# Optimization experiments

Measured on AMD Instinct MI355X. Metric: run time of the kernel, lower is better.

Reference implementation:

```python
import jax, jax.numpy as jnp
import numpy as np

E = 8            # n_expert
K = 2            # n_expert_per_token
C = 2048         # n_embd
I = 1408         # moe_intermediate_size
IS = I * 2       # shared expert intermediate (n_shared_expert=2)
B, T = 2, 2048


def setup_inputs() -> dict:
    key = jax.random.key(0)
    ks = jax.random.split(key, 9)
    s = 0.02
    return {
        "x": jax.random.normal(ks[0], (B, T, C), dtype=jnp.float32),
        "gate_w": jax.random.normal(ks[1], (E, C), dtype=jnp.float32) * s,
        # expert MLP weights, torch Linear convention (out_features, in_features)
        "w1": jax.random.normal(ks[2], (E, I, C), dtype=jnp.float32) * s,  # fc_1
        "w2": jax.random.normal(ks[3], (E, I, C), dtype=jnp.float32) * s,  # fc_2
        "w3": jax.random.normal(ks[4], (E, C, I), dtype=jnp.float32) * s,  # proj
        # shared expert
        "sw1": jax.random.normal(ks[5], (IS, C), dtype=jnp.float32) * s,
        "sw2": jax.random.normal(ks[6], (IS, C), dtype=jnp.float32) * s,
        "sw3": jax.random.normal(ks[7], (C, IS), dtype=jnp.float32) * s,
    }


def reference(x, gate_w, w1, w2, w3, sw1, sw2, sw3):
    Bq, Tq, Cq = x.shape
    xf = x.reshape(-1, Cq)  # [N, C], N = B*T

    # top-k routing: softmax in fp32, then top-k probs per token
    logits = xf @ gate_w.T                                   # [N, E]
    probs = jax.nn.softmax(logits.astype(jnp.float32), axis=-1)
    topk_p, topk_i = jax.lax.top_k(probs, K)                 # [N, K]
    # combine weights: comb[n, e] = sum_k topk_p[n,k] * (topk_i[n,k] == e)
    comb = (jax.nn.one_hot(topk_i, E, dtype=jnp.float32)
            * topk_p[..., None]).sum(axis=1).astype(x.dtype)  # [N, E]

    # per-expert gated-SiLU MLP (batched over experts via einsum)
    h1 = jnp.einsum('nc,eic->eni', xf, w1)                   # [E, N, I]
    h2 = jnp.einsum('nc,eic->eni', xf, w2)                   # [E, N, I]
    h = jax.nn.silu(h1) * h2
    eo = jnp.einsum('eni,eci->enc', h, w3)                   # [E, N, C]

    # weighted scatter-combine
    y = jnp.einsum('enc,ne->nc', eo, comb).reshape(Bq, Tq, Cq)

    # shared expert on the residual input
    sh = (jax.nn.silu(xf @ sw1.T) * (xf @ sw2.T)) @ sw3.T    # [N, C]
    return y + sh.reshape(Bq, Tq, Cq)
```

## Files before the change

kernel.cpp:

```cpp
#include <hip/hip_runtime.h>
#include <stdint.h>

#define N_TOK 4096
#define CDIM  2048
#define NEXP  8
#define IDIM  1408
#define ISDIM 2816
#define CAP   2048
#define ICAT  2816
#define SCAT  5632

typedef __attribute__((ext_vector_type(8))) short bf16x8;
typedef __attribute__((ext_vector_type(4))) float f32x4;

#define GLOAD16(gp, lp) __builtin_amdgcn_global_load_lds( \
    (const __attribute__((address_space(1))) void*)(gp),  \
    (__attribute__((address_space(3))) void*)(lp), 16, 0, 0)

__device__ __forceinline__ unsigned short f2bf(float f) {
  union { float f; unsigned u; } c; c.f = f;
  return (unsigned short)((c.u + 0x7FFFu + ((c.u >> 16) & 1u)) >> 16);
}
__device__ __forceinline__ float bf2f(unsigned short h) {
  union { unsigned u; float f; } c; c.u = (unsigned)h << 16;
  return c.f;
}

__device__ __forceinline__ int xcd_swizzle(int orig, int nwg) {
  int q = nwg >> 3, r = nwg & 7;
  int xcd = orig & 7, idx = orig >> 3;
  return (xcd < r ? xcd * (q + 1) : r * (q + 1) + (xcd - r) * q) + idx;
}

__global__ __launch_bounds__(256) void cvt_all(
    const float* __restrict__ x, const float* __restrict__ w1,
    const float* __restrict__ w2, const float* __restrict__ w3,
    const float* __restrict__ sw1, const float* __restrict__ sw2,
    const float* __restrict__ sw3,
    unsigned short* __restrict__ xb, unsigned short* __restrict__ wcat,
    unsigned short* __restrict__ w3b, unsigned short* __restrict__ swcat,
    unsigned short* __restrict__ sw3b) {
  const int b = blockIdx.x;
  const int t = threadIdx.x;
  const float* src;
  unsigned short* dst;
  if (b < 4096) {
    src = x + (size_t)b * 2048;  dst = xb + (size_t)b * 2048;
  } else if (b < 15360) {
    size_t o = (size_t)(b - 4096) * 2048;  src = w3 + o;  dst = w3b + o;
  } else if (b < 18176) {
    size_t o = (size_t)(b - 15360) * 2048; src = sw3 + o; dst = sw3b + o;
  } else if (b < 40704) {
    int g = b - 18176;
    int e = g / 2816, r = g - e * 2816;
    int dr;
    if (r < 1408) { src = w1 + ((size_t)e * 1408 + r) * 2048; dr = (r >> 7) * 256 + (r & 127); }
    else { int r2 = r - 1408; src = w2 + ((size_t)e * 1408 + r2) * 2048; dr = (r2 >> 7) * 256 + 128 + (r2 & 127); }
    dst = wcat + ((size_t)e * ICAT + dr) * 2048;
  } else {
    int g = b - 40704;
    int dr;
    if (g < 2816) {
      int zn = g >= 1408, rr = g - zn * 1408;
      src = sw1 + (size_t)g * 2048;
      dr = zn * 2816 + (rr >> 7) * 256 + (rr & 127);
    } else {
      int r = g - 2816;
      int zn = r >= 1408, rr = r - zn * 1408;
      src = sw2 + (size_t)r * 2048;
      dr = zn * 2816 + (rr >> 7) * 256 + 128 + (rr & 127);
    }
    dst = swcat + (size_t)dr * 2048;
  }
  size_t i = (size_t)t * 8;
  float4 v0 = *(const float4*)(src + i);
  float4 v1 = *(const float4*)(src + i + 4);
  bf16x8 o;
  o[0] = (short)f2bf(v0.x); o[1] = (short)f2bf(v0.y);
  o[2] = (short)f2bf(v0.z); o[3] = (short)f2bf(v0.w);
  o[4] = (short)f2bf(v1.x); o[5] = (short)f2bf(v1.y);
  o[6] = (short)f2bf(v1.z); o[7] = (short)f2bf(v1.w);
  *(bf16x8*)(dst + i) = o;
}

__global__ __launch_bounds__(64) void routing_kernel(
    const float* __restrict__ x, const float* __restrict__ gw,
    int* __restrict__ counts, int* __restrict__ list,
    int* __restrict__ slot_of, float* __restrict__ wts) {
  const int n = blockIdx.x;
  const int lane = threadIdx.x;
  const float* xr = x + (size_t)n * CDIM;
  float s[NEXP];
#pragma unroll
  for (int e = 0; e < NEXP; e++) s[e] = 0.f;
  for (int c = lane; c < CDIM; c += 64) {
    float xv = xr[c];
#pragma unroll
    for (int e = 0; e < NEXP; e++) s[e] += xv * gw[e * CDIM + c];
  }
#pragma unroll
  for (int e = 0; e < NEXP; e++) {
    float v = s[e];
    for (int o = 32; o > 0; o >>= 1) v += __shfl_down(v, o);
    s[e] = v;
  }
  if (lane == 0) {
    float mx = s[0];
#pragma unroll
    for (int e = 1; e < NEXP; e++) mx = fmaxf(mx, s[e]);
    float p[NEXP], sum = 0.f;
#pragma unroll
    for (int e = 0; e < NEXP; e++) { p[e] = __expf(s[e] - mx); sum += p[e]; }
    int i0 = 0;
#pragma unroll
    for (int e = 1; e < NEXP; e++) if (p[e] > p[i0]) i0 = e;
    int i1 = (i0 == 0) ? 1 : 0;
#pragma unroll
    for (int e = 0; e < NEXP; e++) if (e != i0 && p[e] > p[i1]) i1 = e;
    float inv = 1.f / sum;
    int s0 = atomicAdd(&counts[i0], 1);
    int s1 = atomicAdd(&counts[i1], 1);
    if (s0 < CAP) list[i0 * CAP + s0] = n; else s0 = 0;
    if (s1 < CAP) list[i1 * CAP + s1] = n; else s1 = 0;
    slot_of[n * 2]     = i0 * CAP + s0;
    slot_of[n * 2 + 1] = i1 * CAP + s1;
    wts[n * 2]     = p[i0] * inv;
    wts[n * 2 + 1] = p[i1] * inv;
  }
}

template <int PHASE>
__global__ __launch_bounds__(512) void moe_gemm(
    const unsigned short* __restrict__ xb,
    const unsigned short* __restrict__ swcat,
    const unsigned short* __restrict__ wcat,
    unsigned short* __restrict__ hs_out,
    unsigned short* __restrict__ he_out,
    const unsigned short* __restrict__ hs,
    const unsigned short* __restrict__ sw3b,
    const unsigned short* __restrict__ he,
    const unsigned short* __restrict__ w3b,
    float* __restrict__ ysf,
    unsigned short* __restrict__ eo,
    const int* __restrict__ list,
    const int* __restrict__ counts) {
  const int z = blockIdx.z;
  const unsigned short *A, *B;
  unsigned short* O = nullptr;
  float* Of = nullptr;
  int Ka, ldo;
  int cnt = 1 << 30;
  const int* lst = nullptr;
  int Mt, Nt;
  bool gath = false;
  if (PHASE == 1) {
    Mt = 8; Nt = 11; Ka = CDIM;
    if (z < 4) {
      int zm = z >> 1, zn = z & 1;
      A = xb + (size_t)zm * 2048 * CDIM;
      B = swcat + (size_t)zn * 2816 * CDIM;
      O = hs_out + (size_t)zm * 2048 * ISDIM + (size_t)zn * 1408;
      ldo = ISDIM;
    } else {
      int e = z - 4;
      cnt = counts[e]; if (cnt > CAP) cnt = CAP;
      lst = list + e * CAP;
      gath = true;
      A = xb;
      B = wcat + (size_t)e * ICAT * CDIM;
      O = he_out + (size_t)e * CAP * IDIM;
      ldo = IDIM;
    }
  } else {
    Mt = 8; Nt = 8;
    if (z < 2) {
      Ka = ISDIM;
      A = hs + (size_t)z * 2048 * ISDIM;
      B = sw3b;
      Of = ysf + (size_t)z * 2048 * CDIM;
      ldo = CDIM;
    } else {
      int e = z - 2;
      cnt = counts[e]; if (cnt > CAP) cnt = CAP;
      Ka = IDIM;
      A = he + (size_t)e * CAP * IDIM;
      B = w3b + (size_t)e * CDIM * IDIM;
      O = eo + (size_t)e * CAP * CDIM;
      ldo = CDIM;
    }
  }
  const int wg = xcd_swizzle(blockIdx.x, Mt * Nt);
  const int mt = wg % Mt, nt = wg / Mt;
  if (mt * 256 >= cnt) return;

  __shared__ __align__(16) char lds[3][32768];

  const int tid = threadIdx.x;
  const int srow = tid >> 2;
  const int c16  = (tid & 3) << 4;
  const int scol = c16 ^ (((srow >> 1) & 3) << 4);
  const char *aS0, *aS1, *bS0, *bS1;
  {
    int ar0 = mt * 256 + srow;
    int ar1 = mt * 256 + 128 + srow;
    if (PHASE == 1 && gath) {
      ar0 = (ar0 < cnt) ? lst[ar0] : lst[0];
      ar1 = (ar1 < cnt) ? lst[ar1] : lst[0];
    }
    aS0 = (const char*)A + (size_t)ar0 * Ka * 2 + scol;
    aS1 = (const char*)A + (size_t)ar1 * Ka * 2 + scol;
    bS0 = (const char*)B + (size_t)(nt * 256 + srow) * Ka * 2 + scol;
    bS1 = (const char*)B + (size_t)(nt * 256 + 128 + srow) * Ka * 2 + scol;
  }
  auto stage = [&](int buf, int kt) {
    size_t kb = (size_t)kt * 64;
    char* d = &lds[buf][0] + tid * 16;
    GLOAD16(aS0 + kb, d);
    GLOAD16(aS1 + kb, d + 8192);
    GLOAD16(bS0 + kb, d + 16384);
    GLOAD16(bS1 + kb, d + 24576);
  };

  const int lane = tid & 63, wid = tid >> 6;
  const int wr = wid >> 2, wc = wid & 3;
  const int lrow = lane & 15;
  const int klane = (lane >> 4) << 4;
  const int rsw = ((lrow >> 1) & 3) << 4;
  const int aOff = (wr * 128 + lrow) * 64 + (klane ^ rsw);
  const int bOff = 16384 + (wc * 64 + lrow) * 64 + (klane ^ rsw);

  f32x4 acc[8][4];
#pragma unroll
  for (int mf = 0; mf < 8; mf++)
#pragma unroll
    for (int nf = 0; nf < 4; nf++) acc[mf][nf] = (f32x4){0.f, 0.f, 0.f, 0.f};

  stage(0, 0);
  stage(1, 1);

  const int ntk = Ka >> 5;
  int cur = 0, nx2 = 2;
  for (int t = 0; t < ntk; t++) {
    if (t + 1 < ntk) asm volatile("s_waitcnt vmcnt(4)" ::: "memory");
    else             asm volatile("s_waitcnt vmcnt(0)" ::: "memory");
    __builtin_amdgcn_s_barrier();
    const char* base = lds[cur];
    bf16x8 aR[8], bR[4];
#pragma unroll
    for (int i = 0; i < 8; i++) aR[i] = *(const bf16x8*)(base + aOff + i * 1024);
#pragma unroll
    for (int i = 0; i < 4; i++) bR[i] = *(const bf16x8*)(base + bOff + i * 1024);
    if (t + 2 < ntk) stage(nx2, t + 2);
    __builtin_amdgcn_s_setprio(1);
#pragma unroll
    for (int nf = 0; nf < 4; nf++)
#pragma unroll
      for (int mf = 0; mf < 8; mf++)
        acc[mf][nf] = __builtin_amdgcn_mfma_f32_16x16x32_bf16(
            aR[mf], bR[nf], acc[mf][nf], 0, 0, 0);
    __builtin_amdgcn_s_setprio(0);
    cur = (cur == 2) ? 0 : cur + 1;
    nx2 = (nx2 == 2) ? 0 : nx2 + 1;
  }

  const int r4 = (lane >> 4) * 4;
  if (PHASE == 1) {
    __syncthreads();
    unsigned short* ldsH = (unsigned short*)&lds[0][0];
    if (wc >= 2) {
      const int cb = (wc - 2) * 64;
#pragma unroll
      for (int mf = 0; mf < 8; mf++)
#pragma unroll
        for (int nf = 0; nf < 4; nf++) {
          int cc = cb + nf * 16 + lrow;
#pragma unroll
          for (int r = 0; r < 4; r++) {
            int rr = wr * 128 + mf * 16 + r4 + r;
            ldsH[rr * 128 + (cc ^ (((rr >> 2) & 7) << 4))] = f2bf(acc[mf][nf][r]);
          }
        }
    }
    __syncthreads();
    if (wc < 2) {
      const int cb = wc * 64;
#pragma unroll
      for (int mf = 0; mf < 8; mf++) {
#pragma unroll
        for (int nf = 0; nf < 4; nf++) {
          int cc = cb + nf * 16 + lrow;
          int col = nt * 128 + cc;
#pragma unroll
          for (int r = 0; r < 4; r++) {
            int rr = wr * 128 + mf * 16 + r4 + r;
            float z1 = acc[mf][nf][r];
            float z2 = bf2f(ldsH[rr * 128 + (cc ^ (((rr >> 2) & 7) << 4))]);
            float gv = z1 / (1.f + __expf(-z1)) * z2;
            O[(size_t)(mt * 256 + rr) * ldo + col] = f2bf(gv);
          }
        }
      }
    }
  } else {
    const int rowb = mt * 256 + wr * 128;
    const int colb = nt * 256 + wc * 64;
#pragma unroll
    for (int mf = 0; mf < 8; mf++) {
      int row0 = rowb + mf * 16 + r4;
#pragma unroll
      for (int nf = 0; nf < 4; nf++) {
        int col = colb + nf * 16 + lrow;
#pragma unroll
        for (int r = 0; r < 4; r++) {
          if (z < 2)
            Of[(size_t)(row0 + r) * ldo + col] = acc[mf][nf][r];
          else
            O[(size_t)(row0 + r) * ldo + col] = f2bf(acc[mf][nf][r]);
        }
      }
    }
  }
}

__global__ __launch_bounds__(256) void combine_kernel(
    float* __restrict__ y, const float* __restrict__ ysf,
    const unsigned short* __restrict__ eo,
    const int* __restrict__ slot_of, const float* __restrict__ wts) {
  int idx = blockIdx.x * 256 + threadIdx.x;
  int n = idx >> 9;
  int c = (idx & 511) * 4;
  float4 v = *(const float4*)(ysf + (size_t)n * CDIM + c);
#pragma unroll
  for (int k = 0; k < 2; k++) {
    int slot = slot_of[n * 2 + k];
    float w = wts[n * 2 + k];
    ushort4 h = *(const ushort4*)(eo + (size_t)slot * CDIM + c);
    v.x += w * bf2f(h.x);
    v.y += w * bf2f(h.y);
    v.z += w * bf2f(h.z);
    v.w += w * bf2f(h.w);
  }
  *(float4*)(y + (size_t)n * CDIM + c) = v;
}

extern "C" void kernel_launch(void* const* d_in, const int* in_sizes, int n_in,
                              void* d_out, int out_size, void* d_ws, size_t ws_size,
                              hipStream_t stream) {
  const float* x   = (const float*)d_in[0];
  const float* gw  = (const float*)d_in[1];
  const float* w1  = (const float*)d_in[2];
  const float* w2  = (const float*)d_in[3];
  const float* w3  = (const float*)d_in[4];
  const float* sw1 = (const float*)d_in[5];
  const float* sw2 = (const float*)d_in[6];
  const float* sw3 = (const float*)d_in[7];
  float* y = (float*)d_out;

  char* ws = (char*)d_ws;
  size_t off = 0;
  auto alloc = [&](size_t b) -> void* {
    void* p = ws + off;
    off += (b + 255) & ~(size_t)255;
    return p;
  };
  unsigned short* xb    = (unsigned short*)alloc((size_t)N_TOK * CDIM * 2);
  unsigned short* wcat  = (unsigned short*)alloc((size_t)NEXP * ICAT * CDIM * 2);
  unsigned short* w3b   = (unsigned short*)alloc((size_t)NEXP * CDIM * IDIM * 2);
  unsigned short* swcat = (unsigned short*)alloc((size_t)SCAT * CDIM * 2);
  unsigned short* sw3b  = (unsigned short*)alloc((size_t)CDIM * ISDIM * 2);
  unsigned short* hs    = (unsigned short*)alloc((size_t)N_TOK * ISDIM * 2);
  unsigned short* he    = (unsigned short*)alloc((size_t)NEXP * CAP * IDIM * 2);
  float*          ysf   = (float*)alloc((size_t)N_TOK * CDIM * 4);
  int*   counts  = (int*)alloc(NEXP * 4);
  int*   list    = (int*)alloc((size_t)NEXP * CAP * 4);
  int*   slot_of = (int*)alloc((size_t)N_TOK * 2 * 4);
  float* wtsb    = (float*)alloc((size_t)N_TOK * 2 * 4);
  unsigned short* eoB = wcat;

  hipMemsetAsync(counts, 0, NEXP * 4, stream);
  routing_kernel<<<N_TOK, 64, 0, stream>>>(x, gw, counts, list, slot_of, wtsb);

  cvt_all<<<46336, 256, 0, stream>>>(x, w1, w2, w3, sw1, sw2, sw3,
                                     xb, wcat, w3b, swcat, sw3b);

  moe_gemm<1><<<dim3(88, 1, 12), 512, 0, stream>>>(
      xb, swcat, wcat, hs, he, hs, sw3b, he, w3b, ysf, eoB, list, counts);

  moe_gemm<2><<<dim3(64, 1, 10), 512, 0, stream>>>(
      xb, swcat, wcat, hs, he, hs, sw3b, he, w3b, ysf, eoB, list, counts);

  combine_kernel<<<(N_TOK * (CDIM / 4)) / 256, 256, 0, stream>>>(y, ysf, eoB, slot_of, wtsb);
}
```

Measured before the change: 596.5 us.

## Convert MoE GEMMs to persistent kernels with atomic work-queue tile scheduling

```diff
diff --git a/kernel.cpp b/kernel.cpp
--- a/kernel.cpp
+++ b/kernel.cpp
@@ -24,12 +24,6 @@
 __device__ __forceinline__ float bf2f(unsigned short h) {
   union { unsigned u; float f; } c; c.u = (unsigned)h << 16;
   return c.f;
-}
-
-__device__ __forceinline__ int xcd_swizzle(int orig, int nwg) {
-  int q = nwg >> 3, r = nwg & 7;
-  int xcd = orig & 7, idx = orig >> 3;
-  return (xcd < r ? xcd * (q + 1) : r * (q + 1) + (xcd - r) * q) + idx;
 }
 
 __global__ __launch_bounds__(256) void cvt_all(
@@ -143,84 +137,15 @@
     float* __restrict__ ysf,
     unsigned short* __restrict__ eo,
     const int* __restrict__ list,
-    const int* __restrict__ counts) {
-  const int z = blockIdx.z;
-  const unsigned short *A, *B;
-  unsigned short* O = nullptr;
-  float* Of = nullptr;
-  int Ka, ldo;
-  int cnt = 1 << 30;
-  const int* lst = nullptr;
-  int Mt, Nt;
-  bool gath = false;
-  if (PHASE == 1) {
-    Mt = 8; Nt = 11; Ka = CDIM;
-    if (z < 4) {
-      int zm = z >> 1, zn = z & 1;
-      A = xb + (size_t)zm * 2048 * CDIM;
-      B = swcat + (size_t)zn * 2816 * CDIM;
-      O = hs_out + (size_t)zm * 2048 * ISDIM + (size_t)zn * 1408;
-      ldo = ISDIM;
-    } else {
-      int e = z - 4;
-      cnt = counts[e]; if (cnt > CAP) cnt = CAP;
-      lst = list + e * CAP;
-      gath = true;
-      A = xb;
-      B = wcat + (size_t)e * ICAT * CDIM;
-      O = he_out + (size_t)e * CAP * IDIM;
-      ldo = IDIM;
-    }
-  } else {
-    Mt = 8; Nt = 8;
-    if (z < 2) {
-      Ka = ISDIM;
-      A = hs + (size_t)z * 2048 * ISDIM;
-      B = sw3b;
-      Of = ysf + (size_t)z * 2048 * CDIM;
-      ldo = CDIM;
-    } else {
-      int e = z - 2;
-      cnt = counts[e]; if (cnt > CAP) cnt = CAP;
-      Ka = IDIM;
-      A = he + (size_t)e * CAP * IDIM;
-      B = w3b + (size_t)e * CDIM * IDIM;
-      O = eo + (size_t)e * CAP * CDIM;
-      ldo = CDIM;
-    }
-  }
-  const int wg = xcd_swizzle(blockIdx.x, Mt * Nt);
-  const int mt = wg % Mt, nt = wg / Mt;
-  if (mt * 256 >= cnt) return;
-
+    const int* __restrict__ counts,
+    int* __restrict__ ctr) {
   __shared__ __align__(16) char lds[3][32768];
+  __shared__ int s_w;
 
   const int tid = threadIdx.x;
   const int srow = tid >> 2;
   const int c16  = (tid & 3) << 4;
   const int scol = c16 ^ (((srow >> 1) & 3) << 4);
-  const char *aS0, *aS1, *bS0, *bS1;
-  {
-    int ar0 = mt * 256 + srow;
-    int ar1 = mt * 256 + 128 + srow;
-    if (PHASE == 1 && gath) {
-      ar0 = (ar0 < cnt) ? lst[ar0] : lst[0];
-      ar1 = (ar1 < cnt) ? lst[ar1] : lst[0];
-    }
-    aS0 = (const char*)A + (size_t)ar0 * Ka * 2 + scol;
-    aS1 = (const char*)A + (size_t)ar1 * Ka * 2 + scol;
-    bS0 = (const char*)B + (size_t)(nt * 256 + srow) * Ka * 2 + scol;
-    bS1 = (const char*)B + (size_t)(nt * 256 + 128 + srow) * Ka * 2 + scol;
-  }
-  auto stage = [&](int buf, int kt) {
-    size_t kb = (size_t)kt * 64;
-    char* d = &lds[buf][0] + tid * 16;
-    GLOAD16(aS0 + kb, d);
-    GLOAD16(aS1 + kb, d + 8192);
-    GLOAD16(bS0 + kb, d + 16384);
-    GLOAD16(bS1 + kb, d + 24576);
-  };
-
   const int lane = tid & 63, wid = tid >> 6;
   const int wr = wid >> 2, wc = wid & 3;
   const int lrow = lane & 15;
@@ -228,94 +153,172 @@
   const int rsw = ((lrow >> 1) & 3) << 4;
   const int aOff = (wr * 128 + lrow) * 64 + (klane ^ rsw);
   const int bOff = 16384 + (wc * 64 + lrow) * 64 + (klane ^ rsw);
-
-  f32x4 acc[8][4];
-#pragma unroll
-  for (int mf = 0; mf < 8; mf++)
-#pragma unroll
-    for (int nf = 0; nf < 4; nf++) acc[mf][nf] = (f32x4){0.f, 0.f, 0.f, 0.f};
-
-  stage(0, 0);
-  stage(1, 1);
-
-  const int ntk = Ka >> 5;
-  int cur = 0, nx2 = 2;
-  for (int t = 0; t < ntk; t++) {
-    if (t + 1 < ntk) asm volatile("s_waitcnt vmcnt(4)" ::: "memory");
-    else             asm volatile("s_waitcnt vmcnt(0)" ::: "memory");
-    __builtin_amdgcn_s_barrier();
-    const char* base = lds[cur];
-    bf16x8 aR[8], bR[4];
-#pragma unroll
-    for (int i = 0; i < 8; i++) aR[i] = *(const bf16x8*)(base + aOff + i * 1024);
-#pragma unroll
-    for (int i = 0; i < 4; i++) bR[i] = *(const bf16x8*)(base + bOff + i * 1024);
-    if (t + 2 < ntk) stage(nx2, t + 2);
-    __builtin_amdgcn_s_setprio(1);
-#pragma unroll
-    for (int nf = 0; nf < 4; nf++)
-#pragma unroll
-      for (int mf = 0; mf < 8; mf++)
-        acc[mf][nf] = __builtin_amdgcn_mfma_f32_16x16x32_bf16(
-            aR[mf], bR[nf], acc[mf][nf], 0, 0, 0);
-    __builtin_amdgcn_s_setprio(0);
-    cur = (cur == 2) ? 0 : cur + 1;
-    nx2 = (nx2 == 2) ? 0 : nx2 + 1;
-  }
-
   const int r4 = (lane >> 4) * 4;
-  if (PHASE == 1) {
+  const int TOT = (PHASE == 1) ? 12 * 88 : 10 * 64;
+
+  for (;;) {
+    if (tid == 0) s_w = atomicAdd(ctr, 1);
     __syncthreads();
-    unsigned short* ldsH = (unsigned short*)&lds[0][0];
-    if (wc >= 2) {
-      const int cb = (wc - 2) * 64;
-#pragma unroll
-      for (int mf = 0; mf < 8; mf++)
-#pragma unroll
-        for (int nf = 0; nf < 4; nf++) {
-          int cc = cb + nf * 16 + lrow;
-#pragma unroll
-          for (int r = 0; r < 4; r++) {
-            int rr = wr * 128 + mf * 16 + r4 + r;
-            ldsH[rr * 128 + (cc ^ (((rr >> 2) & 7) << 4))] = f2bf(acc[mf][nf][r]);
+    const int w = s_w;
+    if (w >= TOT) break;
+    int z, mt, nt;
+    if (PHASE == 1) { z = w / 88; int r = w - z * 88; mt = r & 7; nt = r >> 3; }
+    else            { z = w / 64; int r = w - z * 64; mt = r & 7; nt = r >> 3; }
+
+    const unsigned short *A, *B;
+    unsigned short* O = nullptr;
+    float* Of = nullptr;
+    int Ka, ldo;
+    int cnt = 1 << 30;
+    const int* lst = nullptr;
+    bool gath = false;
+    if (PHASE == 1) {
+      Ka = CDIM;
+      if (z < 4) {
+        int zm = z >> 1, zn = z & 1;
+        A = xb + (size_t)zm * 2048 * CDIM;
+        B = swcat + (size_t)zn * 2816 * CDIM;
+        O = hs_out + (size_t)zm * 2048 * ISDIM + (size_t)zn * 1408;
+        ldo = ISDIM;
+      } else {
+        int e = z - 4;
+        cnt = counts[e]; if (cnt > CAP) cnt = CAP;
+        lst = list + e * CAP;
+        gath = true;
+        A = xb;
+        B = wcat + (size_t)e * ICAT * CDIM;
+        O = he_out + (size_t)e * CAP * IDIM;
+        ldo = IDIM;
+      }
+    } else {
+      if (z < 2) {
+        Ka = ISDIM;
+        A = hs + (size_t)z * 2048 * ISDIM;
+        B = sw3b;
+        Of = ysf + (size_t)z * 2048 * CDIM;
+        ldo = CDIM;
+      } else {
+        int e = z - 2;
+        cnt = counts[e]; if (cnt > CAP) cnt = CAP;
+        Ka = IDIM;
+        A = he + (size_t)e * CAP * IDIM;
+        B = w3b + (size_t)e * CDIM * IDIM;
+        O = eo + (size_t)e * CAP * CDIM;
+        ldo = CDIM;
+      }
+    }
+    if (mt * 256 >= cnt) continue;
+
+    const char *aS0, *aS1, *bS0, *bS1;
+    {
+      int ar0 = mt * 256 + srow;
+      int ar1 = mt * 256 + 128 + srow;
+      if (PHASE == 1 && gath) {
+        ar0 = (ar0 < cnt) ? lst[ar0] : lst[0];
+        ar1 = (ar1 < cnt) ? lst[ar1] : lst[0];
+      }
+      aS0 = (const char*)A + (size_t)ar0 * Ka * 2 + scol;
+      aS1 = (const char*)A + (size_t)ar1 * Ka * 2 + scol;
+      bS0 = (const char*)B + (size_t)(nt * 256 + srow) * Ka * 2 + scol;
+      bS1 = (const char*)B + (size_t)(nt * 256 + 128 + srow) * Ka * 2 + scol;
+    }
+    auto stage = [&](int buf, int kt) {
+      size_t kb = (size_t)kt * 64;
+      char* d = &lds[buf][0] + tid * 16;
+      GLOAD16(aS0 + kb, d);
+      GLOAD16(aS1 + kb, d + 8192);
+      GLOAD16(bS0 + kb, d + 16384);
+      GLOAD16(bS1 + kb, d + 24576);
+    };
+
+    f32x4 acc[8][4];
+#pragma unroll
+    for (int mf = 0; mf < 8; mf++)
+#pragma unroll
+      for (int nf = 0; nf < 4; nf++) acc[mf][nf] = (f32x4){0.f, 0.f, 0.f, 0.f};
+
+    stage(0, 0);
+    stage(1, 1);
+
+    const int ntk = Ka >> 5;
+    int cur = 0, nx2 = 2;
+    for (int t = 0; t < ntk; t++) {
+      if (t + 1 < ntk) asm volatile("s_waitcnt vmcnt(4)" ::: "memory");
+      else             asm volatile("s_waitcnt vmcnt(0)" ::: "memory");
+      __builtin_amdgcn_s_barrier();
+      const char* base = lds[cur];
+      bf16x8 aR[8], bR[4];
+#pragma unroll
+      for (int i = 0; i < 8; i++) aR[i] = *(const bf16x8*)(base + aOff + i * 1024);
+#pragma unroll
+      for (int i = 0; i < 4; i++) bR[i] = *(const bf16x8*)(base + bOff + i * 1024);
+      if (t + 2 < ntk) stage(nx2, t + 2);
+      __builtin_amdgcn_s_setprio(1);
+#pragma unroll
+      for (int nf = 0; nf < 4; nf++)
+#pragma unroll
+        for (int mf = 0; mf < 8; mf++)
+          acc[mf][nf] = __builtin_amdgcn_mfma_f32_16x16x32_bf16(
+              aR[mf], bR[nf], acc[mf][nf], 0, 0, 0);
+      __builtin_amdgcn_s_setprio(0);
+      cur = (cur == 2) ? 0 : cur + 1;
+      nx2 = (nx2 == 2) ? 0 : nx2 + 1;
+    }
+
+    if (PHASE == 1) {
+      __syncthreads();
+      unsigned short* ldsH = (unsigned short*)&lds[0][0];
+      if (wc >= 2) {
+        const int cb = (wc - 2) * 64;
+#pragma unroll
+        for (int mf = 0; mf < 8; mf++)
+#pragma unroll
+          for (int nf = 0; nf < 4; nf++) {
+            int cc = cb + nf * 16 + lrow;
+#pragma unroll
+            for (int r = 0; r < 4; r++) {
+              int rr = wr * 128 + mf * 16 + r4 + r;
+              ldsH[rr * 128 + (cc ^ (((rr >> 2) & 7) << 4))] = f2bf(acc[mf][nf][r]);
+            }
+          }
+      }
+      __syncthreads();
+      if (wc < 2) {
+        const int cb = wc * 64;
+#pragma unroll
+        for (int mf = 0; mf < 8; mf++) {
+#pragma unroll
+          for (int nf = 0; nf < 4; nf++) {
+            int cc = cb + nf * 16 + lrow;
+            int col = nt * 128 + cc;
+#pragma unroll
+            for (int r = 0; r < 4; r++) {
+              int rr = wr * 128 + mf * 16 + r4 + r;
+              float z1 = acc[mf][nf][r];
+              float z2 = bf2f(ldsH[rr * 128 + (cc ^ (((rr >> 2) & 7) << 4))]);
+              float gv = z1 / (1.f + __expf(-z1)) * z2;
+              O[(size_t)(mt * 256 + rr) * ldo + col] = f2bf(gv);
+            }
           }
         }
-    }
-    __syncthreads();
-    if (wc < 2) {
-      const int cb = wc * 64;
+      }
+      __syncthreads();
+    } else {
+      const int rowb = mt * 256 + wr * 128;
+      const int colb = nt * 256 + wc * 64;
 #pragma unroll
       for (int mf = 0; mf < 8; mf++) {
+        int row0 = rowb + mf * 16 + r4;
 #pragma unroll
         for (int nf = 0; nf < 4; nf++) {
-          int cc = cb + nf * 16 + lrow;
-          int col = nt * 128 + cc;
+          int col = colb + nf * 16 + lrow;
 #pragma unroll
           for (int r = 0; r < 4; r++) {
-            int rr = wr * 128 + mf * 16 + r4 + r;
-            float z1 = acc[mf][nf][r];
-            float z2 = bf2f(ldsH[rr * 128 + (cc ^ (((rr >> 2) & 7) << 4))]);
-            float gv = z1 / (1.f + __expf(-z1)) * z2;
-            O[(size_t)(mt * 256 + rr) * ldo + col] = f2bf(gv);
+            if (z < 2)
+              Of[(size_t)(row0 + r) * ldo + col] = acc[mf][nf][r];
+            else
+              O[(size_t)(row0 + r) * ldo + col] = f2bf(acc[mf][nf][r]);
           }
-        }
-      }
-    }
-  } else {
-    const int rowb = mt * 256 + wr * 128;
-    const int colb = nt * 256 + wc * 64;
-#pragma unroll
-    for (int mf = 0; mf < 8; mf++) {
-      int row0 = rowb + mf * 16 + r4;
-#pragma unroll
-      for (int nf = 0; nf < 4; nf++) {
-        int col = colb + nf * 16 + lrow;
-#pragma unroll
-        for (int r = 0; r < 4; r++) {
-          if (z < 2)
-            Of[(size_t)(row0 + r) * ldo + col] = acc[mf][nf][r];
-          else
-            O[(size_t)(row0 + r) * ldo + col] = f2bf(acc[mf][nf][r]);
         }
       }
     }
@@ -375,19 +378,21 @@
   int*   list    = (int*)alloc((size_t)NEXP * CAP * 4);
   int*   slot_of = (int*)alloc((size_t)N_TOK * 2 * 4);
   float* wtsb    = (float*)alloc((size_t)N_TOK * 2 * 4);
+  int*   ctrs    = (int*)alloc(2 * 4);
   unsigned short* eoB = wcat;
 
   hipMemsetAsync(counts, 0, NEXP * 4, stream);
+  hipMemsetAsync(ctrs, 0, 2 * 4, stream);
   routing_kernel<<<N_TOK, 64, 0, stream>>>(x, gw, counts, list, slot_of, wtsb);
 
   cvt_all<<<46336, 256, 0, stream>>>(x, w1, w2, w3, sw1, sw2, sw3,
                                      xb, wcat, w3b, swcat, sw3b);
 
-  moe_gemm<1><<<dim3(88, 1, 12), 512, 0, stream>>>(
-      xb, swcat, wcat, hs, he, hs, sw3b, he, w3b, ysf, eoB, list, counts);
-
-  moe_gemm<2><<<dim3(64, 1, 10), 512, 0, stream>>>(
-      xb, swcat, wcat, hs, he, hs, sw3b, he, w3b, ysf, eoB, list, counts);
+  moe_gemm<1><<<dim3(256, 1, 1), 512, 0, stream>>>(
+      xb, swcat, wcat, hs, he, hs, sw3b, he, w3b, ysf, eoB, list, counts, ctrs + 0);
+
+  moe_gemm<2><<<dim3(256, 1, 1), 512, 0, stream>>>(
+      xb, swcat, wcat, hs, he, hs, sw3b, he, w3b, ysf, eoB, list, counts, ctrs + 1);
 
   combine_kernel<<<(N_TOK * (CDIM / 4)) / 256, 256, 0, stream>>>(y, ysf, eoB, slot_of, wtsb);
 }
```

After: 596.0 us. No clear change (-0.1%).
